# Kernel tuning notes

Measured on AMD Instinct MI355X. Metric: run time of the kernel, lower is better.

Reference implementation:

```python
import jax, jax.numpy as jnp
import numpy as np

N_NODES = 50000


def gcn_conv(x, src, dst, W, b, n_nodes):
    """PyG GCNConv: linear -> sym-normalized aggregation with self-loops -> bias."""
    h = x @ W  # [N, out]
    # add self loops
    loop = jnp.arange(n_nodes, dtype=src.dtype)
    src_f = jnp.concatenate([src, loop])
    dst_f = jnp.concatenate([dst, loop])
    # degree at target nodes (edge weight = 1)
    deg = jax.ops.segment_sum(jnp.ones_like(dst_f, dtype=h.dtype), dst_f, num_segments=n_nodes)
    dinv = jnp.where(deg > 0, jax.lax.rsqrt(deg), 0.0)
    norm = dinv[src_f] * dinv[dst_f]  # [E+N]
    msg = h[src_f] * norm[:, None]    # gather + scale
    out = jax.ops.segment_sum(msg, dst_f, num_segments=n_nodes)
    return out + b


def setup_inputs() -> dict:
    key = jax.random.key(0)
    k1, k2, k3, k4 = jax.random.split(key, 4)
    N, F, H, C, E = N_NODES, 512, 256, 16, 800000
    x = jax.random.normal(k1, (N, F), dtype=jnp.float32)
    edge_index = jax.random.randint(k2, (2, E), 0, N, dtype=jnp.int64)
    W1 = jax.random.normal(k3, (F, H), dtype=jnp.float32) * (1.0 / np.sqrt(F))
    b1 = jnp.zeros((H,), dtype=jnp.float32)
    W2 = jax.random.normal(k4, (H, C), dtype=jnp.float32) * (1.0 / np.sqrt(H))
    b2 = jnp.zeros((C,), dtype=jnp.float32)
    return {"x": x, "edge_index": edge_index, "W1": W1, "b1": b1, "W2": W2, "b2": b2}


def reference(x, edge_index, W1, b1, W2, b2):
    src, dst = edge_index[0], edge_index[1]
    h = gcn_conv(x, src, dst, W1, b1, N_NODES)
    h = jax.nn.relu(h)
    # F.dropout with training=False (eval mode) is identity
    out = gcn_conv(h, src, dst, W2, b2, N_NODES)
    return out
```

## Files before the change

kernel.cpp:

```cpp
#include <hip/hip_runtime.h>
#include <stdint.h>

#define N_NODES 50000
#define N_PAD   50048
#define F_IN 512
#define H_DIM 256
#define C_DIM 16

typedef __attribute__((ext_vector_type(8))) short short8;
typedef __attribute__((ext_vector_type(4))) float f32x4;
typedef __attribute__((ext_vector_type(4))) unsigned short us4;
typedef __attribute__((ext_vector_type(8))) unsigned short us8;

__device__ inline float bf2f(unsigned short u) {
    return __uint_as_float(((uint32_t)u) << 16);
}
__device__ inline unsigned short f2bf(float f) {
    uint32_t u = __float_as_uint(f);
    u += 0x7FFFu + ((u >> 16) & 1u);
    return (unsigned short)(u >> 16);
}
__device__ inline unsigned short hx(float f) {
    return (unsigned short)(__float_as_uint(f) >> 16);
}
__device__ inline int eidx(const void* p, long long i, int is64) {
    return is64 ? (int)((const long long*)p)[i] : ((const int*)p)[i];
}

#define GLOAD16(gp, lp)                                                       \
    __builtin_amdgcn_global_load_lds(                                         \
        (const __attribute__((address_space(1))) void*)(gp),                  \
        (__attribute__((address_space(3))) void*)(lp), 16, 0, 0)


__global__ void prep_k(const void* ei, int* flag,
                       const float* w1, unsigned short* w1t,
                       const float* w2, unsigned short* w2t,
                       int* cnt, int* cur) {
    int i = blockIdx.x * 256 + threadIdx.x;
    if (i == 0) {
        const uint32_t* w = (const uint32_t*)ei;
        int is64 = 1;
        for (int j = 1; j < 128; j += 2)
            if (w[j] != 0u) { is64 = 0; break; }
        *flag = is64;
    }
    if (i < N_NODES) { cnt[i] = 0; cur[i] = 0; }
    if (i < F_IN * H_DIM) {
        int k = i / H_DIM, n = i % H_DIM;
        w1t[n * F_IN + k] = f2bf(w1[i]);
    }
    if (i < H_DIM * C_DIM) {
        int k = i / C_DIM, n = i % C_DIM;
        w2t[n * H_DIM + k] = f2bf(w2[i]);
    }
}


__global__ void hist_k(const void* ei, const int* flag, int* cnt, long long E) {
    long long e = (long long)blockIdx.x * 256 + threadIdx.x;
    if (e >= E) return;
    int d = eidx(ei, E + e, *flag);
    atomicAdd(&cnt[d], 1);
}

__global__ __launch_bounds__(512) void scan1_k(const int* cnt, int* rowoff, int* bsum,
                                               float* dinv, int n) {
    __shared__ int s[512];
    int t = threadIdx.x;
    int i = blockIdx.x * 512 + t;
    int v = (i < n) ? cnt[i] : 0;
    s[t] = v;
    __syncthreads();
    for (int off = 1; off < 512; off <<= 1) {
        int add = (t >= off) ? s[t - off] : 0;
        __syncthreads();
        s[t] += add;
        __syncthreads();
    }
    if (i < n) {
        rowoff[i] = s[t] - v;
        dinv[i] = rsqrtf((float)(v + 1));
    }
    if (t == 511) bsum[blockIdx.x] = s[511];
}

__global__ void scan2_k(int* bsum, int nb) {
    __shared__ int s[128];
    int t = threadIdx.x;
    int v = (t < nb) ? bsum[t] : 0;
    s[t] = v;
    __syncthreads();
    for (int off = 1; off < 128; off <<= 1) {
        int add = (t >= off) ? s[t - off] : 0;
        __syncthreads();
        s[t] += add;
        __syncthreads();
    }
    if (t < nb) bsum[t] = s[t] - v;
}

__global__ __launch_bounds__(512) void scan3_k(int* rowoff, const int* bsum, int n, int total) {
    int i = blockIdx.x * 512 + threadIdx.x;
    if (i < n) rowoff[i] += bsum[blockIdx.x];
    if (i == 0) rowoff[n] = total;
}

__global__ void scatter_k(const void* ei, const int* flag, const float* dinv,
                          const int* rowoff, int* cur, long long E, int2* colnorm) {
    long long e = (long long)blockIdx.x * 256 + threadIdx.x;
    if (e >= E) return;
    int is64 = *flag;
    int s = eidx(ei, e, is64);
    int d = eidx(ei, E + e, is64);
    int pos = rowoff[d] + atomicAdd(&cur[d], 1);
    float nrm = dinv[s] * dinv[d];
    int2 cn;
    cn.x = s;
    cn.y = __float_as_int(nrm);
    colnorm[pos] = cn;
}


__global__ __launch_bounds__(512, 4) void gemm1_k(const float* __restrict__ x,
                                                  const unsigned short* __restrict__ w1t,
                                                  unsigned short* __restrict__ h1) {
    __shared__ __align__(16) float          Asf[2][128 * 32];
    __shared__ __align__(16) unsigned short Bs[2][256 * 32];

    const int t = threadIdx.x;
    const int wv = t >> 6, lane = t & 63;
    const int lg = lane >> 4, lr = lane & 15;
    const int wm = wv >> 2, wn = wv & 3;

    const int arow0 = t >> 3;
    const int achk = (t & 7) ^ (arow0 & 7);
    size_t g0 = (size_t)blockIdx.x * 128 + arow0;
    size_t g1 = g0 + 64;
    if (g0 > N_NODES - 1) g0 = N_NODES - 1;
    if (g1 > N_NODES - 1) g1 = N_NODES - 1;
    const float* asrc0 = x + g0 * F_IN + achk * 4;
    const float* asrc1 = x + g1 * F_IN + achk * 4;
    const unsigned short* bsrc0 = w1t + (size_t)(t >> 2) * F_IN + (t & 3) * 8;
    const unsigned short* bsrc1 = bsrc0 + 128 * F_IN;

#define STAGE(bf, ks)                                                         \
    do { const int _o = (ks) * 32;                                            \
        GLOAD16(asrc0 + _o, &Asf[bf][t * 4]);                                 \
        GLOAD16(asrc1 + _o, &Asf[bf][t * 4 + 2048]);                          \
        GLOAD16(bsrc0 + _o, &Bs[bf][t * 8]);                                  \
        GLOAD16(bsrc1 + _o, &Bs[bf][(t + 512) * 8]);                          \
    } while (0)

    f32x4 acc[4][4] = {};

    STAGE(0, 0);
    __syncthreads();

    for (int ks = 0; ks < 16; ++ks) {
        const int bf = ks & 1;
        if (ks < 15) STAGE(bf ^ 1, ks + 1);
        short8 afr[4], bfr[4];
#pragma unroll
        for (int mi = 0; mi < 4; ++mi) {
            const int r = wm * 64 + mi * 16 + lr;
            const int s = r & 7;
            const float* base = &Asf[bf][r * 32];
            f32x4 lo = *(const f32x4*)(base + (((lg * 2) ^ s) * 4));
            f32x4 hi = *(const f32x4*)(base + (((lg * 2 + 1) ^ s) * 4));
            short8 a;
            a[0] = (short)hx(lo[0]); a[1] = (short)hx(lo[1]);
            a[2] = (short)hx(lo[2]); a[3] = (short)hx(lo[3]);
            a[4] = (short)hx(hi[0]); a[5] = (short)hx(hi[1]);
            a[6] = (short)hx(hi[2]); a[7] = (short)hx(hi[3]);
            afr[mi] = a;
        }
#pragma unroll
        for (int ni = 0; ni < 4; ++ni)
            bfr[ni] = *(const short8*)&Bs[bf][(wn * 64 + ni * 16 + lr) * 32 + lg * 8];
#pragma unroll
        for (int mi = 0; mi < 4; ++mi)
#pragma unroll
            for (int ni = 0; ni < 4; ++ni)
                acc[mi][ni] = __builtin_amdgcn_mfma_f32_16x16x32_bf16(
                    afr[mi], bfr[ni], acc[mi][ni], 0, 0, 0);
        __syncthreads();
    }
#undef STAGE

    const size_t rbase = (size_t)blockIdx.x * 128 + wm * 64 + lg * 4;
#pragma unroll
    for (int mi = 0; mi < 4; ++mi)
#pragma unroll
        for (int ni = 0; ni < 4; ++ni)
#pragma unroll
            for (int j = 0; j < 4; ++j)
                h1[(rbase + mi * 16 + j) * H_DIM + wn * 64 + ni * 16 + lr] =
                    f2bf(acc[mi][ni][j]);
}


__global__ __launch_bounds__(256) void agg1_k(const unsigned short* __restrict__ h1,
                                              const int* __restrict__ rowoff,
                                              const int2* __restrict__ colnorm,
                                              const float* __restrict__ dinv,
                                              const float* __restrict__ b1,
                                              unsigned short* __restrict__ h1a) {
    int wv = threadIdx.x >> 6, lane = threadIdx.x & 63;
    int node = blockIdx.x * 4 + wv;
    if (node >= N_NODES) return;
    int half = lane >> 5;
    int fl = (lane & 31) * 8;
    int beg = rowoff[node], end = rowoff[node + 1];
    float a[8] = {0.f, 0.f, 0.f, 0.f, 0.f, 0.f, 0.f, 0.f};
    const unsigned short* base = h1 + fl;

    int e = beg + half;
    while (e + 6 < end) {
        int2 c[4];
        us8 v[4];
#pragma unroll
        for (int q = 0; q < 4; ++q) c[q] = colnorm[e + q * 2];
#pragma unroll
        for (int q = 0; q < 4; ++q)
            v[q] = *(const us8*)(base + (long long)c[q].x * H_DIM);
#pragma unroll
        for (int q = 0; q < 4; ++q) {
            float n = __int_as_float(c[q].y);
#pragma unroll
            for (int j = 0; j < 8; ++j) a[j] += n * bf2f(v[q][j]);
        }
        e += 8;
    }
    while (e < end) {
        int2 c0 = colnorm[e];
        us8 v0 = *(const us8*)(base + (long long)c0.x * H_DIM);
        float n0 = __int_as_float(c0.y);
#pragma unroll
        for (int j = 0; j < 8; ++j) a[j] += n0 * bf2f(v0[j]);
        e += 2;
    }
#pragma unroll
    for (int j = 0; j < 8; ++j)
        a[j] += __shfl_xor(a[j], 32);

    if (half == 0) {
        float dn = dinv[node];
        float sn = dn * dn;
        us8 vs = *(const us8*)(base + (long long)node * H_DIM);
        float4 b0 = *(const float4*)(b1 + fl);
        float4 b4 = *(const float4*)(b1 + fl + 4);
        float bb[8] = {b0.x, b0.y, b0.z, b0.w, b4.x, b4.y, b4.z, b4.w};
        us8 o;
#pragma unroll
        for (int j = 0; j < 8; ++j) {
            float r = fmaxf(a[j] + sn * bf2f(vs[j]) + bb[j], 0.f);
            o[j] = f2bf(r);
        }
        *(us8*)(h1a + (long long)node * H_DIM + fl) = o;
    }
}


__global__ __launch_bounds__(256) void gemm2_k(const unsigned short* __restrict__ h1a,
                                               const unsigned short* __restrict__ w2t,
                                               float* __restrict__ h2) {
    int t = threadIdx.x;
    int wv = t >> 6, lane = t & 63, lg = lane >> 4, lr = lane & 15;
    int rbase = blockIdx.x * 64 + wv * 16;
    int rr = rbase + lr;
    int rc = rr < N_NODES ? rr : N_NODES - 1;
    f32x4 acc = {0.f, 0.f, 0.f, 0.f};
#pragma unroll
    for (int ks = 0; ks < 8; ++ks) {
        short8 a = *(const short8*)(h1a + (long long)rc * H_DIM + ks * 32 + lg * 8);
        short8 b = *(const short8*)(w2t + lr * H_DIM + ks * 32 + lg * 8);
        acc = __builtin_amdgcn_mfma_f32_16x16x32_bf16(a, b, acc, 0, 0, 0);
    }
#pragma unroll
    for (int j = 0; j < 4; ++j) {
        int row = rbase + lg * 4 + j;
        if (row < N_NODES) h2[(long long)row * C_DIM + lr] = acc[j];
    }
}


__global__ __launch_bounds__(256) void agg2_k(const float* __restrict__ h2,
                                              const int* __restrict__ rowoff,
                                              const int2* __restrict__ colnorm,
                                              const float* __restrict__ dinv,
                                              const float* __restrict__ b2,
                                              float* __restrict__ out) {
    int g = threadIdx.x >> 4, c = threadIdx.x & 15;
    int node = blockIdx.x * 16 + g;
    if (node >= N_NODES) return;
    int beg = rowoff[node], end = rowoff[node + 1];
    float acc = 0.f;
    int e = beg;
    for (; e + 1 < end; e += 2) {
        int2 cn0 = colnorm[e];
        int2 cn1 = colnorm[e + 1];
        acc += __int_as_float(cn0.y) * h2[(long long)cn0.x * C_DIM + c]
             + __int_as_float(cn1.y) * h2[(long long)cn1.x * C_DIM + c];
    }
    if (e < end) {
        int2 cn = colnorm[e];
        acc += __int_as_float(cn.y) * h2[(long long)cn.x * C_DIM + c];
    }
    float dn = dinv[node];
    acc += dn * dn * h2[(long long)node * C_DIM + c];
    out[(long long)node * C_DIM + c] = acc + b2[c];
}


extern "C" void kernel_launch(void* const* d_in, const int* in_sizes, int n_in,
                              void* d_out, int out_size, void* d_ws, size_t ws_size,
                              hipStream_t stream) {
    const float* x  = (const float*)d_in[0];
    const void*  ei = d_in[1];
    const float* W1 = (const float*)d_in[2];
    const float* b1 = (const float*)d_in[3];
    const float* W2 = (const float*)d_in[4];
    const float* b2 = (const float*)d_in[5];
    float* out = (float*)d_out;
    long long E = (long long)in_sizes[1] / 2;

    char* w = (char*)d_ws;
    auto alloc = [&](size_t bytes) -> char* {
        char* p = w;
        w += (bytes + 255) & ~(size_t)255;
        return p;
    };
    int*   flag    = (int*)   alloc(4);
    int*   cnt     = (int*)   alloc((size_t)N_NODES * 4);
    int*   cur     = (int*)   alloc((size_t)N_NODES * 4);
    float* dinv    = (float*) alloc((size_t)N_NODES * 4);
    int*   rowoff  = (int*)   alloc((size_t)(N_NODES + 1) * 4);
    int*   bsum    = (int*)   alloc(512 * 4);
    int2*  colnorm = (int2*)  alloc((size_t)E * 8);
    unsigned short* w1t = (unsigned short*)alloc((size_t)H_DIM * F_IN * 2);
    unsigned short* w2t = (unsigned short*)alloc((size_t)C_DIM * H_DIM * 2);
    unsigned short* h1  = (unsigned short*)alloc((size_t)N_PAD * H_DIM * 2);
    unsigned short* h1a = (unsigned short*)alloc((size_t)N_NODES * H_DIM * 2);
    float* h2 = (float*)alloc((size_t)N_NODES * C_DIM * 4);

    prep_k<<<(F_IN * H_DIM + 255) / 256, 256, 0, stream>>>(ei, flag, W1, w1t, W2, w2t,
                                                           cnt, cur);

    int egrid = (int)((E + 255) / 256);
    hist_k<<<egrid, 256, 0, stream>>>(ei, flag, cnt, E);
    int sgrid = (N_NODES + 511) / 512;
    scan1_k<<<sgrid, 512, 0, stream>>>(cnt, rowoff, bsum, dinv, N_NODES);
    scan2_k<<<1, 128, 0, stream>>>(bsum, sgrid);
    scan3_k<<<sgrid, 512, 0, stream>>>(rowoff, bsum, N_NODES, (int)E);
    scatter_k<<<egrid, 256, 0, stream>>>(ei, flag, dinv, rowoff, cur, E, colnorm);

    gemm1_k<<<N_PAD / 128, 512, 0, stream>>>(x, w1t, h1);
    agg1_k<<<(N_NODES + 3) / 4, 256, 0, stream>>>(h1, rowoff, colnorm, dinv, b1, h1a);
    gemm2_k<<<(N_NODES + 63) / 64, 256, 0, stream>>>(h1a, w2t, h2);
    agg2_k<<<(N_NODES + 15) / 16, 256, 0, stream>>>(h2, rowoff, colnorm, dinv, b2, out);
}
```

Baseline: 210.7 us.

## Drop scan3 kernel, fold block offsets into readers, tighten gemm1 waits, unroll agg2

Removes the third scan pass by having scatter, agg1 and agg2 add the per-block prefix sum on the fly when reading row offsets, which saves one kernel launch and a pass over rowoff. The gemm1 loop replaces __syncthreads with explicit vmcnt/lgkmcnt waits plus raw barriers, so the next stage's async LDS loads can stay in flight while the current tile is consumed. agg2 also unrolls its edge loop to four, issuing more independent gathers. The cost is an extra bsum load per row lookup, and the hand-written waitcnt values depend on exactly four global loads being issued per stage.

```diff
diff --git a/kernel.cpp b/kernel.cpp
--- a/kernel.cpp
+++ b/kernel.cpp
@@ -25,6 +25,13 @@
 }
 __device__ inline int eidx(const void* p, long long i, int is64) {
     return is64 ? (int)((const long long*)p)[i] : ((const int*)p)[i];
+}
+
+__device__ inline int row_beg(const int* ro, const int* bs, int n) {
+    return ro[n] + bs[n >> 9];
+}
+__device__ inline int row_end(const int* ro, const int* bs, int n, int E) {
+    return (n + 1 < N_NODES) ? ro[n + 1] + bs[(n + 1) >> 9] : E;
 }
 
 #define GLOAD16(gp, lp)                                                       \
@@ -100,20 +107,15 @@
     if (t < nb) bsum[t] = s[t] - v;
 }
 
-__global__ __launch_bounds__(512) void scan3_k(int* rowoff, const int* bsum, int n, int total) {
-    int i = blockIdx.x * 512 + threadIdx.x;
-    if (i < n) rowoff[i] += bsum[blockIdx.x];
-    if (i == 0) rowoff[n] = total;
-}
-
 __global__ void scatter_k(const void* ei, const int* flag, const float* dinv,
-                          const int* rowoff, int* cur, long long E, int2* colnorm) {
+                          const int* rowoff, const int* bsum, int* cur,
+                          long long E, int2* colnorm) {
     long long e = (long long)blockIdx.x * 256 + threadIdx.x;
     if (e >= E) return;
     int is64 = *flag;
     int s = eidx(ei, e, is64);
     int d = eidx(ei, E + e, is64);
-    int pos = rowoff[d] + atomicAdd(&cur[d], 1);
+    int pos = row_beg(rowoff, bsum, d) + atomicAdd(&cur[d], 1);
     float nrm = dinv[s] * dinv[d];
     int2 cn;
     cn.x = s;
@@ -155,11 +157,18 @@
     f32x4 acc[4][4] = {};
 
     STAGE(0, 0);
-    __syncthreads();
 
     for (int ks = 0; ks < 16; ++ks) {
         const int bf = ks & 1;
-        if (ks < 15) STAGE(bf ^ 1, ks + 1);
+        if (ks < 15) {
+            STAGE(bf ^ 1, ks + 1);
+            asm volatile("s_waitcnt vmcnt(4)" ::: "memory");
+        } else {
+            asm volatile("s_waitcnt vmcnt(0)" ::: "memory");
+        }
+        __builtin_amdgcn_sched_barrier(0);
+        __builtin_amdgcn_s_barrier();
+
         short8 afr[4], bfr[4];
 #pragma unroll
         for (int mi = 0; mi < 4; ++mi) {
@@ -184,7 +193,10 @@
             for (int ni = 0; ni < 4; ++ni)
                 acc[mi][ni] = __builtin_amdgcn_mfma_f32_16x16x32_bf16(
                     afr[mi], bfr[ni], acc[mi][ni], 0, 0, 0);
-        __syncthreads();
+
+        asm volatile("s_waitcnt lgkmcnt(0)" ::: "memory");
+        __builtin_amdgcn_sched_barrier(0);
+        __builtin_amdgcn_s_barrier();
     }
 #undef STAGE
 
@@ -202,16 +214,19 @@
 
 __global__ __launch_bounds__(256) void agg1_k(const unsigned short* __restrict__ h1,
                                               const int* __restrict__ rowoff,
+                                              const int* __restrict__ bsum,
                                               const int2* __restrict__ colnorm,
                                               const float* __restrict__ dinv,
                                               const float* __restrict__ b1,
-                                              unsigned short* __restrict__ h1a) {
+                                              unsigned short* __restrict__ h1a,
+                                              int E) {
     int wv = threadIdx.x >> 6, lane = threadIdx.x & 63;
     int node = blockIdx.x * 4 + wv;
     if (node >= N_NODES) return;
     int half = lane >> 5;
     int fl = (lane & 31) * 8;
-    int beg = rowoff[node], end = rowoff[node + 1];
+    int beg = row_beg(rowoff, bsum, node);
+    int end = row_end(rowoff, bsum, node, E);
     float a[8] = {0.f, 0.f, 0.f, 0.f, 0.f, 0.f, 0.f, 0.f};
     const unsigned short* base = h1 + fl;
 
@@ -287,23 +302,31 @@
 
 __global__ __launch_bounds__(256) void agg2_k(const float* __restrict__ h2,
                                               const int* __restrict__ rowoff,
+                                              const int* __restrict__ bsum,
                                               const int2* __restrict__ colnorm,
                                               const float* __restrict__ dinv,
                                               const float* __restrict__ b2,
-                                              float* __restrict__ out) {
+                                              float* __restrict__ out, int E) {
     int g = threadIdx.x >> 4, c = threadIdx.x & 15;
     int node = blockIdx.x * 16 + g;
     if (node >= N_NODES) return;
-    int beg = rowoff[node], end = rowoff[node + 1];
+    int beg = row_beg(rowoff, bsum, node);
+    int end = row_end(rowoff, bsum, node, E);
     float acc = 0.f;
     int e = beg;
-    for (; e + 1 < end; e += 2) {
+    for (; e + 3 < end; e += 4) {
         int2 cn0 = colnorm[e];
         int2 cn1 = colnorm[e + 1];
-        acc += __int_as_float(cn0.y) * h2[(long long)cn0.x * C_DIM + c]
-             + __int_as_float(cn1.y) * h2[(long long)cn1.x * C_DIM + c];
-    }
-    if (e < end) {
+        int2 cn2 = colnorm[e + 2];
+        int2 cn3 = colnorm[e + 3];
+        float v0 = h2[(long long)cn0.x * C_DIM + c];
+        float v1 = h2[(long long)cn1.x * C_DIM + c];
+        float v2 = h2[(long long)cn2.x * C_DIM + c];
+        float v3 = h2[(long long)cn3.x * C_DIM + c];
+        acc += __int_as_float(cn0.y) * v0 + __int_as_float(cn1.y) * v1
+             + __int_as_float(cn2.y) * v2 + __int_as_float(cn3.y) * v3;
+    }
+    for (; e < end; ++e) {
         int2 cn = colnorm[e];
         acc += __int_as_float(cn.y) * h2[(long long)cn.x * C_DIM + c];
     }
@@ -335,7 +358,7 @@
     int*   cnt     = (int*)   alloc((size_t)N_NODES * 4);
     int*   cur     = (int*)   alloc((size_t)N_NODES * 4);
     float* dinv    = (float*) alloc((size_t)N_NODES * 4);
-    int*   rowoff  = (int*)   alloc((size_t)(N_NODES + 1) * 4);
+    int*   rowoff  = (int*)   alloc((size_t)N_NODES * 4);
     int*   bsum    = (int*)   alloc(512 * 4);
     int2*  colnorm = (int2*)  alloc((size_t)E * 8);
     unsigned short* w1t = (unsigned short*)alloc((size_t)H_DIM * F_IN * 2);
@@ -352,11 +375,12 @@
     int sgrid = (N_NODES + 511) / 512;
     scan1_k<<<sgrid, 512, 0, stream>>>(cnt, rowoff, bsum, dinv, N_NODES);
     scan2_k<<<1, 128, 0, stream>>>(bsum, sgrid);
-    scan3_k<<<sgrid, 512, 0, stream>>>(rowoff, bsum, N_NODES, (int)E);
-    scatter_k<<<egrid, 256, 0, stream>>>(ei, flag, dinv, rowoff, cur, E, colnorm);
+    scatter_k<<<egrid, 256, 0, stream>>>(ei, flag, dinv, rowoff, bsum, cur, E, colnorm);
 
     gemm1_k<<<N_PAD / 128, 512, 0, stream>>>(x, w1t, h1);
-    agg1_k<<<(N_NODES + 3) / 4, 256, 0, stream>>>(h1, rowoff, colnorm, dinv, b1, h1a);
+    agg1_k<<<(N_NODES + 3) / 4, 256, 0, stream>>>(h1, rowoff, bsum, colnorm, dinv,
+                                                  b1, h1a, (int)E);
     gemm2_k<<<(N_NODES + 63) / 64, 256, 0, stream>>>(h1a, w2t, h2);
-    agg2_k<<<(N_NODES + 15) / 16, 256, 0, stream>>>(h2, rowoff, colnorm, dinv, b2, out);
-}
+    agg2_k<<<(N_NODES + 15) / 16, 256, 0, stream>>>(h2, rowoff, bsum, colnorm, dinv,
+                                                    b2, out, (int)E);
+}
```

Result: faster. 202.2 us (-4.0%).
